# Kernel tuning notes

Hardware: AMD Instinct MI355X
Metric: run time of the kernel (lower is better)

## Reference

```python
import jax, jax.numpy as jnp
import numpy as np

B, TV, TL = 4, 13600, 256
VD, LD, E, H = 256, 768, 256, 8
HD = E // H
SCALE = HD ** -0.5
CLAMP = 50000.0
NEG = -9e15


def _xavier(k, out_d, in_d):
    lim = np.sqrt(6.0 / (in_d + out_d)).astype(np.float32)
    return jax.random.uniform(k, (out_d, in_d), minval=-lim, maxval=lim, dtype=jnp.float32)


def setup_inputs() -> dict:
    key = jax.random.key(0)
    ks = jax.random.split(key, 10)
    return {
        "v": jax.random.normal(ks[0], (B, TV, VD), dtype=jnp.float32),
        "l": jax.random.normal(ks[1], (B, TL, LD), dtype=jnp.float32),
        "v_pos": jax.random.normal(ks[2], (B, TV, VD), dtype=jnp.float32),
        "attention_mask_v": jnp.ones((B, TV), dtype=jnp.float32),
        "attention_mask_l": jnp.ones((B, TL), dtype=jnp.float32),
        "Wq": _xavier(ks[3], E, VD), "bq": jnp.zeros((E,), jnp.float32),
        "Wk": _xavier(ks[4], E, LD), "bk": jnp.zeros((E,), jnp.float32),
        "Wvv": _xavier(ks[5], E, VD), "bvv": jnp.zeros((E,), jnp.float32),
        "Wvl": _xavier(ks[6], E, LD), "bvl": jnp.zeros((E,), jnp.float32),
        "Wov": _xavier(ks[7], VD, E), "bov": jnp.zeros((VD,), jnp.float32),
        "Wol": _xavier(ks[8], LD, E), "bol": jnp.zeros((LD,), jnp.float32),
    }


def _heads(x):  # [B, T, E] -> [B, H, T, HD]
    b, t, _ = x.shape
    return x.reshape(b, t, H, HD).transpose(0, 2, 1, 3)


def reference(v, l, v_pos, attention_mask_v, attention_mask_l,
              Wq, bq, Wk, bk, Wvv, bvv, Wvl, bvl, Wov, bov, Wol, bol):
    # projections (eval mode: dropout disabled)
    q = _heads(((v + v_pos) @ Wq.T + bq) * SCALE)        # [B,H,TV,HD]
    k = _heads(l @ Wk.T + bk)                             # [B,H,TL,HD]
    val_v = _heads(v @ Wvv.T + bvv)                       # [B,H,TV,HD]
    val_l = _heads(l @ Wvl.T + bvl)                       # [B,H,TL,HD]

    # shared scores, computed once: [B,H,TV,TL]
    aw = jnp.einsum('bhtd,bhsd->bhts', q, k)
    aw = jnp.clip(aw, -CLAMP, CLAMP)

    # language-direction scores: transpose, stabilize, clamp
    aw_l = aw.transpose(0, 1, 3, 2)                       # [B,H,TL,TV]
    aw_l = aw_l - jnp.max(aw_l, axis=-1, keepdims=True)
    aw_l = jnp.clip(aw_l, -CLAMP, CLAMP)
    # torch masked_fill(mask==0, NEG) then + : nonzero mask values are ADDED
    mv = jnp.where(attention_mask_v == 0, NEG, attention_mask_v)[:, None, None, :]
    aw_l = aw_l + mv
    p_l = jax.nn.softmax(aw_l, axis=-1)

    # vision-direction scores
    ml = jnp.where(attention_mask_l == 0, NEG, attention_mask_l)[:, None, None, :]
    p_v = jax.nn.softmax(aw + ml, axis=-1)

    out_v = jnp.einsum('bhts,bhsd->bhtd', p_v, val_l)     # [B,H,TV,HD]
    out_l = jnp.einsum('bhst,bhtd->bhsd', p_l, val_v)     # [B,H,TL,HD]
    out_v = out_v.transpose(0, 2, 1, 3).reshape(B, TV, E) @ Wov.T + bov
    out_l = out_l.transpose(0, 2, 1, 3).reshape(B, TL, E) @ Wol.T + bol
    return (out_v, out_l)
```

## Files before the change

kernel.cpp:

```cpp
#include <hip/hip_runtime.h>
#include <math.h>


typedef unsigned short u16;
typedef unsigned int   u32;
typedef __attribute__((ext_vector_type(2))) u32 u32x2;
typedef __attribute__((ext_vector_type(4))) u16 us4;
typedef __attribute__((ext_vector_type(8))) u16 us8;
typedef __attribute__((ext_vector_type(8))) short s8b;
typedef __attribute__((ext_vector_type(4))) float f4;

#define B_   4
#define TV_  13600
#define TL_  256
#define VD_  256
#define LD_  768
#define E_   256
#define H_   8
#define HD_  32
#define PREC 36

static constexpr float SCALE_  = 0.17677669529663687f;
static constexpr float NEG_    = -9e15f;
static constexpr float LOG2E_  = 1.4426950408889634f;

__device__ __forceinline__ float bf2f(u16 x) {
    return __uint_as_float(((u32)x) << 16);
}
__device__ __forceinline__ u16 f2bf(float f) {
    u32 u = __float_as_uint(f);
    u += 0x7fffu + ((u >> 16) & 1u);
    return (u16)(u >> 16);
}
__device__ __forceinline__ u32 cvtpk(float lo, float hi) {
    u32 r;
    asm("v_cvt_pk_bf16_f32 %0, %1, %2" : "=v"(r) : "v"(lo), "v"(hi));
    return r;
}
__device__ __forceinline__ float bflo(u32 w) { return __uint_as_float(w << 16); }
__device__ __forceinline__ float bfhi(u32 w) { return __uint_as_float(w & 0xffff0000u); }

__device__ __forceinline__ s8b frag32(const u16* base, int row, int q) {
    int slot = q ^ ((row >> 1) & 3);
    return *(const s8b*)(base + row * 32 + slot * 8);
}

__global__ void sniff_kernel(const void* __restrict__ mask, int* __restrict__ flag) {
    if (threadIdx.x == 0 && blockIdx.x == 0) {
        u32 w = *(const u32*)mask;
        *flag = (w == 0x3F800000u) ? 1 : 0;
    }
}

__global__ __launch_bounds__(256) void prep_v_kernel(
    const int* __restrict__ flag, const void* __restrict__ v,
    const void* __restrict__ vp, u16* __restrict__ vb, u16* __restrict__ vqb)
{
    const bool f32 = (*flag != 0);
    const size_t n = (size_t)B_ * TV_ * VD_;
    size_t i = ((size_t)blockIdx.x * 256 + threadIdx.x) * 4;
    const size_t stride = (size_t)gridDim.x * 256 * 4;
    for (; i < n; i += stride) {
        float a[4], b[4];
        if (f32) {
            float4 x = ((const float4*)v)[i >> 2];
            float4 y = ((const float4*)vp)[i >> 2];
            a[0]=x.x; a[1]=x.y; a[2]=x.z; a[3]=x.w;
            b[0]=y.x; b[1]=y.y; b[2]=y.z; b[3]=y.w;
        } else {
            us4 x = ((const us4*)v)[i >> 2];
            us4 y = ((const us4*)vp)[i >> 2];
            #pragma unroll
            for (int j = 0; j < 4; ++j) { a[j]=bf2f(x[j]); b[j]=bf2f(y[j]); }
        }
        us4 o1, o2;
        #pragma unroll
        for (int j = 0; j < 4; ++j) { o1[j]=f2bf(a[j]); o2[j]=f2bf(a[j]+b[j]); }
        ((us4*)vb)[i >> 2] = o1;
        ((us4*)vqb)[i >> 2] = o2;
    }
}

struct Seg { const void* src; void* dst; int n; int toF32; };
struct PrepArgs { Seg s[13]; };

__global__ __launch_bounds__(256) void prep_rest_kernel(
    const int* __restrict__ flag, PrepArgs args)
{
    const bool f32 = (*flag != 0);
    for (int k = 0; k < 13; ++k) {
        Seg sg = args.s[k];
        for (int j = blockIdx.x * 256 + threadIdx.x; j < sg.n;
             j += gridDim.x * 256) {
            float x = f32 ? ((const float*)sg.src)[j] : bf2f(((const u16*)sg.src)[j]);
            if (sg.toF32) ((float*)sg.dst)[j] = x;
            else          ((u16*)sg.dst)[j]   = f2bf(x);
        }
    }
}

template<bool CEXT>
__global__ __launch_bounds__(256) void gemm_mfma(
    const int* __restrict__ flag,
    const u16* __restrict__ A, const u16* __restrict__ W,
    const float* __restrict__ bias, void* __restrict__ C, size_t c_off,
    int N, int K, float scale)
{
    __shared__ __align__(16) u16 As[128 * 32];
    __shared__ __align__(16) u16 Bs[128 * 32];
    const int tid  = threadIdx.x;
    const int lane = tid & 63, wid = tid >> 6;
    const int wm = wid >> 1, wn = wid & 1;
    const size_t m0 = (size_t)blockIdx.x * 128;
    const int n0 = blockIdx.y * 128;

    const int srow = tid >> 1;
    const int half = tid & 1;
    const int ssw  = (srow >> 1) & 3;
    const int sl0  = half * 2, sl1 = half * 2 + 1;

    f4 acc[4][4];
    #pragma unroll
    for (int i = 0; i < 4; ++i)
        #pragma unroll
        for (int j = 0; j < 4; ++j) acc[i][j] = (f4){0.f, 0.f, 0.f, 0.f};

    for (int k0 = 0; k0 < K; k0 += 32) {
        {
            const u16* ga = A + (m0 + srow) * (size_t)K + k0;
            *(us8*)&As[srow*32 + sl0*8] = *(const us8*)(ga + (sl0 ^ ssw) * 8);
            *(us8*)&As[srow*32 + sl1*8] = *(const us8*)(ga + (sl1 ^ ssw) * 8);
            const u16* gb = W + ((size_t)(n0 + srow)) * (size_t)K + k0;
            *(us8*)&Bs[srow*32 + sl0*8] = *(const us8*)(gb + (sl0 ^ ssw) * 8);
            *(us8*)&Bs[srow*32 + sl1*8] = *(const us8*)(gb + (sl1 ^ ssw) * 8);
        }
        __syncthreads();
        s8b af[4], bf[4];
        const int q = lane >> 4;
        #pragma unroll
        for (int mt = 0; mt < 4; ++mt)
            af[mt] = frag32(As, wm*64 + mt*16 + (lane & 15), q);
        #pragma unroll
        for (int nt = 0; nt < 4; ++nt)
            bf[nt] = frag32(Bs, wn*64 + nt*16 + (lane & 15), q);
        __builtin_amdgcn_s_setprio(1);
        #pragma unroll
        for (int mt = 0; mt < 4; ++mt)
            #pragma unroll
            for (int nt = 0; nt < 4; ++nt)
                acc[mt][nt] = __builtin_amdgcn_mfma_f32_16x16x32_bf16(
                    af[mt], bf[nt], acc[mt][nt], 0, 0, 0);
        __builtin_amdgcn_s_setprio(0);
        __syncthreads();
    }

    const int q = lane >> 4;
    const bool f32out = CEXT ? (*flag != 0) : false;
    #pragma unroll
    for (int nt = 0; nt < 4; ++nt) {
        const int col = n0 + wn*64 + nt*16 + (lane & 15);
        const float bv = bias[col];
        #pragma unroll
        for (int mt = 0; mt < 4; ++mt) {
            #pragma unroll
            for (int reg = 0; reg < 4; ++reg) {
                const size_t row = m0 + wm*64 + mt*16 + q*4 + reg;
                const float val = (acc[mt][nt][reg] + bv) * scale;
                const size_t idx = c_off + row * (size_t)N + col;
                if (CEXT && f32out) ((float*)C)[idx] = val;
                else                ((u16*)C)[idx]   = f2bf(val);
            }
        }
    }
}

__global__ __launch_bounds__(256, 4) void attn_v_mfma(
    const int* __restrict__ flag,
    const u16* __restrict__ qm, const u16* __restrict__ km,
    const u16* __restrict__ vm, const void* __restrict__ maskl,
    u16* __restrict__ outm)
{
    __shared__ __align__(16) u16 Qs[64 * 32];
    __shared__ __align__(16) u16 Ks[256 * 32];
    __shared__ __align__(16) u16 VTs[32 * 264];
    __shared__ float mls[256];

    const int tid = threadIdx.x, lane = tid & 63, wid = tid >> 6;
    const int bb = blockIdx.z, hh = blockIdx.y;
    const int t0 = blockIdx.x * 64;
    const int q  = lane >> 4;
    const int l15 = lane & 15;

    {
        int row = tid >> 2, slot = tid & 3;
        int sw = (row >> 1) & 3;
        int tg = t0 + row; if (tg >= TV_) tg = TV_ - 1;
        const u16* gp = qm + ((size_t)(bb*TV_ + tg)) * E_ + hh*HD_;
        *(us8*)&Qs[row*32 + slot*8] = *(const us8*)(gp + ((slot ^ sw) * 8));
    }
    {
        int s = tid, sw = (s >> 1) & 3;
        const u16* gp = km + ((size_t)(bb*TL_ + s)) * E_ + hh*HD_;
        #pragma unroll
        for (int slot = 0; slot < 4; ++slot)
            *(us8*)&Ks[s*32 + slot*8] = *(const us8*)(gp + ((slot ^ sw) * 8));
    }
    {
        int s = tid;
        const u16* gp = vm + ((size_t)(bb*TL_ + s)) * E_ + hh*HD_;
        #pragma unroll
        for (int d0 = 0; d0 < 32; d0 += 8) {
            us8 vv = *(const us8*)(gp + d0);
            #pragma unroll
            for (int j = 0; j < 8; ++j) VTs[(d0 + j)*264 + s] = vv[j];
        }
        float mv = (*flag) ? ((const float*)maskl)[(size_t)bb*TL_ + s]
                           : bf2f(((const u16*)maskl)[(size_t)bb*TL_ + s]);
        mls[s] = (mv == 0.0f) ? NEG_ : mv;
    }
    __syncthreads();

    const s8b qf = frag32(Qs, wid*16 + l15, q);
    f4 sacc[16];
    __builtin_amdgcn_s_setprio(1);
    #pragma unroll
    for (int mt = 0; mt < 16; ++mt) {
        s8b kf = frag32(Ks, mt*16 + l15, q);
        f4 z = {0.f, 0.f, 0.f, 0.f};
        sacc[mt] = __builtin_amdgcn_mfma_f32_16x16x32_bf16(kf, qf, z, 0, 0, 0);
    }
    __builtin_amdgcn_s_setprio(0);

    float vmax = -1e30f;
    #pragma unroll
    for (int mt = 0; mt < 16; ++mt) {
        f4 mv4 = *(const f4*)&mls[mt*16 + q*4];
        #pragma unroll
        for (int r = 0; r < 4; ++r) {
            float v = sacc[mt][r] + mv4[r];
            sacc[mt][r] = v;
            vmax = fmaxf(vmax, v);
        }
    }
    vmax = fmaxf(vmax, __shfl_xor(vmax, 16));
    vmax = fmaxf(vmax, __shfl_xor(vmax, 32));

    const float nmL = -vmax * LOG2E_;
    float sum = 0.f;
    u32 pw[32];
    #pragma unroll
    for (int mt = 0; mt < 16; ++mt) {
        float p0 = exp2f(fmaf(sacc[mt][0], LOG2E_, nmL));
        float p1 = exp2f(fmaf(sacc[mt][1], LOG2E_, nmL));
        float p2 = exp2f(fmaf(sacc[mt][2], LOG2E_, nmL));
        float p3 = exp2f(fmaf(sacc[mt][3], LOG2E_, nmL));
        u32 w0 = cvtpk(p0, p1), w1 = cvtpk(p2, p3);
        pw[2*mt]   = w0;
        pw[2*mt+1] = w1;
        sum += bflo(w0) + bfhi(w0) + bflo(w1) + bfhi(w1);
    }
    sum += __shfl_xor(sum, 16);
    sum += __shfl_xor(sum, 32);
    float Lreg[4];
    #pragma unroll
    for (int r = 0; r < 4; ++r) Lreg[r] = __shfl(sum, q*4 + r);

    __syncthreads();

    u16* myP = Ks + wid * (16 * 40);
    f4 oacc[2];
    oacc[0] = (f4){0.f,0.f,0.f,0.f};
    oacc[1] = (f4){0.f,0.f,0.f,0.f};
    __builtin_amdgcn_s_setprio(1);
    #pragma unroll
    for (int ks = 0; ks < 8; ++ks) {
        *(u32x2*)&myP[l15*40 + q*4]      = (u32x2){pw[4*ks],   pw[4*ks+1]};
        *(u32x2*)&myP[l15*40 + 16 + q*4] = (u32x2){pw[4*ks+2], pw[4*ks+3]};
        s8b pa = *(const s8b*)&myP[l15*40 + q*8];
        #pragma unroll
        for (int nt = 0; nt < 2; ++nt) {
            s8b vb = *(const s8b*)&VTs[(nt*16 + l15)*264 + ks*32 + q*8];
            oacc[nt] = __builtin_amdgcn_mfma_f32_16x16x32_bf16(pa, vb, oacc[nt], 0, 0, 0);
        }
    }
    __builtin_amdgcn_s_setprio(0);

    #pragma unroll
    for (int r = 0; r < 4; ++r) {
        const int tg = t0 + wid*16 + q*4 + r;
        if (tg < TV_) {
            const float inv = 1.0f / Lreg[r];
            #pragma unroll
            for (int nt = 0; nt < 2; ++nt)
                outm[((size_t)(bb*TV_ + tg)) * E_ + hh*HD_ + nt*16 + l15] =
                    f2bf(oacc[nt][r] * inv);
        }
    }
}

__global__ __launch_bounds__(256, 8) void attn_l_mfma(
    const int* __restrict__ flag,
    const u16* __restrict__ qm, const u16* __restrict__ km,
    const u16* __restrict__ vm, const void* __restrict__ maskv,
    u16* __restrict__ part, int nchunk, int chunk)
{
    __shared__ __align__(16) u16 smem0[128 * 40];
    __shared__ __align__(16) u16 Qs[32 * 32];
    __shared__ __align__(16) u16 VTs[32 * 32];
    __shared__ float mvs[32];

    const int tid = threadIdx.x, lane = tid & 63, wid = tid >> 6;
    const int bb = blockIdx.z, hh = blockIdx.y;
    const int tc  = blockIdx.x >> 1;
    const int s0b = (blockIdx.x & 1) * 128;
    const int q = lane >> 4, l15 = lane & 15;
    const bool f32m = (*flag != 0);

    {
        int row = tid >> 1, half = tid & 1;
        int sw = (row >> 1) & 3;
        const u16* gp = km + ((size_t)(bb*TL_ + s0b + row)) * E_ + hh*HD_;
        int sl0 = half*2, sl1 = half*2 + 1;
        *(us8*)&smem0[row*32 + sl0*8] = *(const us8*)(gp + ((sl0 ^ sw) * 8));
        *(us8*)&smem0[row*32 + sl1*8] = *(const us8*)(gp + ((sl1 ^ sw) * 8));
    }
    s8b bk0 = frag32(smem0, wid*32 + l15, q);
    s8b bk1 = frag32(smem0, wid*32 + 16 + l15, q);

    float m_s[2], l_s[2];
    f4 oacc[2][2];
    m_s[0] = m_s[1] = -1e30f;
    l_s[0] = l_s[1] = 0.f;
    oacc[0][0] = oacc[0][1] = oacc[1][0] = oacc[1][1] = (f4){0.f,0.f,0.f,0.f};

    const int nstep = chunk >> 5;
    for (int step = 0; step < nstep; ++step) {
        const int t0 = tc * chunk + step * 32;
        if (tid < 128) {
            int row = tid >> 2, slot = tid & 3;
            int sw = (row >> 1) & 3;
            const u16* gp = qm + ((size_t)(bb*TV_ + t0 + row)) * E_ + hh*HD_;
            *(us8*)&Qs[row*32 + slot*8] = *(const us8*)(gp + ((slot ^ sw) * 8));
        } else {
            int t2 = tid - 128;
            int trow = t2 >> 2, d0 = (t2 & 3) * 8;
            us8 vv = *(const us8*)(vm + ((size_t)(bb*TV_ + t0 + trow)) * E_ + hh*HD_ + d0);
            #pragma unroll
            for (int j = 0; j < 8; ++j) {
                int d = d0 + j;
                VTs[d*32 + (((trow >> 3) ^ ((d >> 1) & 3)) * 8) + (trow & 7)] = vv[j];
            }
        }
        if (tid < 32) {
            float mv = f32m ? ((const float*)maskv)[(size_t)bb*TV_ + t0 + tid]
                            : bf2f(((const u16*)maskv)[(size_t)bb*TV_ + t0 + tid]);
            mvs[tid] = (mv == 0.0f) ? NEG_ : mv;
        }
        __syncthreads();

        s8b aq0 = frag32(Qs, l15, q);
        s8b aq1 = frag32(Qs, 16 + l15, q);
        f4 sacc[2][2];
        __builtin_amdgcn_s_setprio(1);
        {
            f4 zz = {0.f, 0.f, 0.f, 0.f};
            sacc[0][0] = __builtin_amdgcn_mfma_f32_16x16x32_bf16(aq0, bk0, zz, 0, 0, 0);
            sacc[0][1] = __builtin_amdgcn_mfma_f32_16x16x32_bf16(aq0, bk1, zz, 0, 0, 0);
            sacc[1][0] = __builtin_amdgcn_mfma_f32_16x16x32_bf16(aq1, bk0, zz, 0, 0, 0);
            sacc[1][1] = __builtin_amdgcn_mfma_f32_16x16x32_bf16(aq1, bk1, zz, 0, 0, 0);
        }
        __builtin_amdgcn_s_setprio(0);

        float mvq[2][4];
        #pragma unroll
        for (int tt = 0; tt < 2; ++tt)
            #pragma unroll
            for (int r = 0; r < 4; ++r) mvq[tt][r] = mvs[tt*16 + q*4 + r];

        #pragma unroll
        for (int st = 0; st < 2; ++st) {
            float v[2][4];
            float vmax = -1e30f;
            #pragma unroll
            for (int tt = 0; tt < 2; ++tt)
                #pragma unroll
                for (int r = 0; r < 4; ++r) {
                    v[tt][r] = sacc[tt][st][r] + mvq[tt][r];
                    vmax = fmaxf(vmax, v[tt][r]);
                }
            vmax = fmaxf(vmax, __shfl_xor(vmax, 16));
            vmax = fmaxf(vmax, __shfl_xor(vmax, 32));
            float m = m_s[st];
            if (__any(vmax > m + 8.0f)) {
                float nm = fmaxf(m, vmax);
                float al = exp2f((m - nm) * LOG2E_);
                l_s[st] *= al;
                #pragma unroll
                for (int dt = 0; dt < 2; ++dt)
                    #pragma unroll
                    for (int r = 0; r < 4; ++r) oacc[dt][st][r] *= al;
                m_s[st] = m = nm;
            }
            const float nmL = -m * LOG2E_;
            const int ls = wid*32 + st*16 + l15;
            float ps = 0.f;
            #pragma unroll
            for (int tt = 0; tt < 2; ++tt) {
                float p0 = exp2f(fmaf(v[tt][0], LOG2E_, nmL));
                float p1 = exp2f(fmaf(v[tt][1], LOG2E_, nmL));
                float p2 = exp2f(fmaf(v[tt][2], LOG2E_, nmL));
                float p3 = exp2f(fmaf(v[tt][3], LOG2E_, nmL));
                u32 w0 = cvtpk(p0, p1), w1 = cvtpk(p2, p3);
                *(u32x2*)&smem0[ls*40 + tt*16 + q*4] = (u32x2){w0, w1};
                ps += bflo(w0) + bfhi(w0) + bflo(w1) + bfhi(w1);
            }
            ps += __shfl_xor(ps, 16);
            ps += __shfl_xor(ps, 32);
            l_s[st] += ps;
        }

        s8b av0 = frag32(VTs, l15, q);
        s8b av1 = frag32(VTs, 16 + l15, q);
        __builtin_amdgcn_s_setprio(1);
        #pragma unroll
        for (int st = 0; st < 2; ++st) {
            s8b bp = *(const s8b*)&smem0[(wid*32 + st*16 + l15)*40 + q*8];
            oacc[0][st] = __builtin_amdgcn_mfma_f32_16x16x32_bf16(av0, bp, oacc[0][st], 0, 0, 0);
            oacc[1][st] = __builtin_amdgcn_mfma_f32_16x16x32_bf16(av1, bp, oacc[1][st], 0, 0, 0);
        }
        __builtin_amdgcn_s_setprio(0);
        __syncthreads();
    }

    #pragma unroll
    for (int st = 0; st < 2; ++st) {
        const int s = s0b + wid*32 + st*16 + l15;
        u16* rec = part + ((size_t)((bb*H_ + hh)*TL_ + s) * nchunk + tc) * PREC;
        #pragma unroll
        for (int dt = 0; dt < 2; ++dt)
            #pragma unroll
            for (int r = 0; r < 4; ++r)
                rec[dt*16 + q*4 + r] = f2bf(oacc[dt][st][r]);
        if (q == 0) {
            *(float*)(rec + 32) = m_s[st];
            *(float*)(rec + 34) = l_s[st];
        }
    }
}

__global__ __launch_bounds__(256) void attn_l_merge(
    const u16* __restrict__ part, u16* __restrict__ outm, int nchunk)
{
    const int R = blockIdx.x * 8 + (threadIdx.x >> 5);
    const int d = threadIdx.x & 31;
    const u16* rec0 = part + (size_t)R * nchunk * PREC;
    float m = -1e30f;
    for (int c = 0; c < nchunk; ++c)
        m = fmaxf(m, *(const float*)(rec0 + c*PREC + 32));
    float L = 0.f, o = 0.f;
    for (int c = 0; c < nchunk; ++c) {
        float mc = *(const float*)(rec0 + c*PREC + 32);
        float lc = *(const float*)(rec0 + c*PREC + 34);
        float w  = exp2f((mc - m) * LOG2E_);
        L += lc * w;
        o += bf2f(rec0[c*PREC + d]) * w;
    }
    o /= L;
    const int bb = R >> 11, hh = (R >> 8) & 7, ss = R & 255;
    outm[(size_t)(bb*TL_ + ss) * E_ + hh*HD_ + d] = f2bf(o);
}

extern "C" void kernel_launch(void* const* d_in, const int* in_sizes, int n_in,
                              void* d_out, int out_size, void* d_ws, size_t ws_size,
                              hipStream_t stream)
{
    const void* v     = d_in[0];
    const void* l     = d_in[1];
    const void* vpos  = d_in[2];
    const void* maskv = d_in[3];
    const void* maskl = d_in[4];
    const void* Wq  = d_in[5];   const void* bq  = d_in[6];
    const void* Wk  = d_in[7];   const void* bk  = d_in[8];
    const void* Wvv = d_in[9];   const void* bvv = d_in[10];
    const void* Wvl = d_in[11];  const void* bvl = d_in[12];
    const void* Wov = d_in[13];  const void* bov = d_in[14];
    const void* Wol = d_in[15];  const void* bol = d_in[16];

    const size_t BIG   = (size_t)B_*TV_*E_*2;
    const size_t TLBUF = (size_t)B_*TL_*E_*2;
    const size_t LBUF  = (size_t)B_*TL_*LD_*2;
    auto part_bytes = [](int nc) { return (size_t)B_*H_*TL_ * (size_t)nc * (PREC*2); };

    const size_t fixed = 512 + 2*(BIG+256) + (LBUF+256) + 3*(TLBUF+256)
                       + (131072+256)*3 + (393216+256)*3 + (8192+256);
    const int cand[3] = {25, 17, 5};
    int nchunk = 5;
    for (int i = 0; i < 3; ++i)
        if (fixed + part_bytes(cand[i]) + 256 <= ws_size) { nchunk = cand[i]; break; }
    const int chunk = TV_ / nchunk;

    char* ws = (char*)d_ws;
    size_t off = 0;
    auto carve = [&](size_t bytes) -> char* {
        char* p = ws + off;
        off += (bytes + 255) & ~(size_t)255;
        return p;
    };
    int*   flag    = (int*)carve(512);
    u16*   slot1   = (u16*)carve(BIG);
    u16*   slot2   = (u16*)carve(BIG);
    u16*   lb      = (u16*)carve(LBUF);
    u16*   k_ws    = (u16*)carve(TLBUF);
    u16*   vall_ws = (u16*)carve(TLBUF);
    u16*   attnl_ws= (u16*)carve(TLBUF);
    u16*   wqb     = (u16*)carve(131072);
    u16*   wkb     = (u16*)carve(393216);
    u16*   wvvb    = (u16*)carve(131072);
    u16*   wvlb    = (u16*)carve(393216);
    u16*   wovb    = (u16*)carve(131072);
    u16*   wolb    = (u16*)carve(393216);
    float* biasf   = (float*)carve(8192);
    u16*   part_ws = (u16*)carve(part_bytes(nchunk));

    u16* vb    = slot1;
    u16* vqb   = slot2;
    u16* valv  = slot2;
    u16* attnv = slot1;
    u16* q_ws  = (u16*)d_out;

    float* bqf  = biasf;        float* bkf  = biasf + 256;
    float* bvvf = biasf + 512;  float* bvlf = biasf + 768;
    float* bovf = biasf + 1024; float* bolf = biasf + 1280;

    const dim3 blk(256);
    const size_t outl_off = (size_t)B_*TV_*VD_;

    sniff_kernel<<<1, 64, 0, stream>>>(maskv, flag);

    prep_v_kernel<<<2048, blk, 0, stream>>>(flag, v, vpos, vb, vqb);
    PrepArgs pa;
    pa.s[0]  = { l,   lb,   B_*TL_*LD_, 0 };
    pa.s[1]  = { Wq,  wqb,  E_*VD_,     0 };
    pa.s[2]  = { Wk,  wkb,  E_*LD_,     0 };
    pa.s[3]  = { Wvv, wvvb, E_*VD_,     0 };
    pa.s[4]  = { Wvl, wvlb, E_*LD_,     0 };
    pa.s[5]  = { Wov, wovb, VD_*E_,     0 };
    pa.s[6]  = { Wol, wolb, LD_*E_,     0 };
    pa.s[7]  = { bq,  bqf,  E_,  1 };
    pa.s[8]  = { bk,  bkf,  E_,  1 };
    pa.s[9]  = { bvv, bvvf, E_,  1 };
    pa.s[10] = { bvl, bvlf, E_,  1 };
    pa.s[11] = { bov, bovf, VD_, 1 };
    pa.s[12] = { bol, bolf, LD_, 1 };
    prep_rest_kernel<<<256, blk, 0, stream>>>(flag, pa);

    gemm_mfma<false><<<dim3(425, 2), blk, 0, stream>>>(flag, vqb, wqb,  bqf,  q_ws,    0, E_, VD_, SCALE_);
    gemm_mfma<false><<<dim3(425, 2), blk, 0, stream>>>(flag, vb,  wvvb, bvvf, valv,    0, E_, VD_, 1.0f);
    gemm_mfma<false><<<dim3(8,   2), blk, 0, stream>>>(flag, lb,  wkb,  bkf,  k_ws,    0, E_, LD_, 1.0f);
    gemm_mfma<false><<<dim3(8,   2), blk, 0, stream>>>(flag, lb,  wvlb, bvlf, vall_ws, 0, E_, LD_, 1.0f);

    attn_l_mfma <<<dim3(nchunk*2, H_, B_), blk, 0, stream>>>(flag, q_ws, k_ws, valv, maskv, part_ws, nchunk, chunk);
    attn_l_merge<<<dim3(B_*H_*TL_/8),      blk, 0, stream>>>(part_ws, attnl_ws, nchunk);
    attn_v_mfma <<<dim3((TV_+63)/64, H_, B_), blk, 0, stream>>>(flag, q_ws, k_ws, vall_ws, maskl, attnv);

    gemm_mfma<true><<<dim3(425, 2), blk, 0, stream>>>(flag, attnv,    wovb, bovf, d_out, 0,        VD_, E_, 1.0f);
    gemm_mfma<true><<<dim3(8,   6), blk, 0, stream>>>(flag, attnl_ws, wolb, bolf, d_out, outl_off, LD_, E_, 1.0f);
}
```

Baseline: 478.1 us.

## Store projections head-major and widen attn_l blocks to all 256 keys

The projection GEMMs now write Q, K and the value tensors in a [B,H,T,HD] head-major layout, so the attention kernels read contiguous 64-byte rows per head instead of strided slices of the E dimension. attn_l_mfma now has each block cover all 256 language rows (four 16-row tiles per wave) instead of splitting them across two blocks. This halves redundant Q/V tile loads, at the cost of more registers and LDS per block and lower occupancy (launch bounds drop from 8 to 4). Partial results are split into a packed bf16 output array and a separate float2 max/sum array laid out chunk-major, so both the stores and the merge reads are coalesced.

Measured after the change: 454.7 us. -4.9%, faster.

```diff
diff --git a/kernel.cpp b/kernel.cpp
--- a/kernel.cpp
+++ b/kernel.cpp
@@ -18,7 +18,7 @@
 #define E_   256
 #define H_   8
 #define HD_  32
-#define PREC 36
+#define NREC (B_*H_*TL_)
 
 static constexpr float SCALE_  = 0.17677669529663687f;
 static constexpr float NEG_    = -9e15f;
@@ -99,7 +99,7 @@
     }
 }
 
-template<bool CEXT>
+template<int OMODE, int TDIM>
 __global__ __launch_bounds__(256) void gemm_mfma(
     const int* __restrict__ flag,
     const u16* __restrict__ A, const u16* __restrict__ W,
@@ -155,7 +155,7 @@
     }
 
     const int q = lane >> 4;
-    const bool f32out = CEXT ? (*flag != 0) : false;
+    const bool f32out = (OMODE == 1) ? (*flag != 0) : false;
     #pragma unroll
     for (int nt = 0; nt < 4; ++nt) {
         const int col = n0 + wn*64 + nt*16 + (lane & 15);
@@ -164,11 +164,17 @@
         for (int mt = 0; mt < 4; ++mt) {
             #pragma unroll
             for (int reg = 0; reg < 4; ++reg) {
-                const size_t row = m0 + wm*64 + mt*16 + q*4 + reg;
+                const int row = (int)m0 + wm*64 + mt*16 + q*4 + reg;
                 const float val = (acc[mt][nt][reg] + bv) * scale;
-                const size_t idx = c_off + row * (size_t)N + col;
-                if (CEXT && f32out) ((float*)C)[idx] = val;
-                else                ((u16*)C)[idx]   = f2bf(val);
+                if (OMODE == 2) {
+                    const int b = row / TDIM, t = row - b * TDIM;
+                    ((u16*)C)[(((size_t)(b*H_ + (col >> 5)))*TDIM + t)*HD_ + (col & 31)]
+                        = f2bf(val);
+                } else {
+                    const size_t idx = c_off + (size_t)row * N + col;
+                    if (f32out) ((float*)C)[idx] = val;
+                    else        ((u16*)C)[idx]   = f2bf(val);
+                }
             }
         }
     }
@@ -187,6 +193,7 @@
 
     const int tid = threadIdx.x, lane = tid & 63, wid = tid >> 6;
     const int bb = blockIdx.z, hh = blockIdx.y;
+    const int bh = bb*H_ + hh;
     const int t0 = blockIdx.x * 64;
     const int q  = lane >> 4;
     const int l15 = lane & 15;
@@ -195,19 +202,19 @@
         int row = tid >> 2, slot = tid & 3;
         int sw = (row >> 1) & 3;
         int tg = t0 + row; if (tg >= TV_) tg = TV_ - 1;
-        const u16* gp = qm + ((size_t)(bb*TV_ + tg)) * E_ + hh*HD_;
+        const u16* gp = qm + ((size_t)(bh*TV_ + tg)) * HD_;
         *(us8*)&Qs[row*32 + slot*8] = *(const us8*)(gp + ((slot ^ sw) * 8));
     }
     {
         int s = tid, sw = (s >> 1) & 3;
-        const u16* gp = km + ((size_t)(bb*TL_ + s)) * E_ + hh*HD_;
+        const u16* gp = km + ((size_t)(bh*TL_ + s)) * HD_;
         #pragma unroll
         for (int slot = 0; slot < 4; ++slot)
             *(us8*)&Ks[s*32 + slot*8] = *(const us8*)(gp + ((slot ^ sw) * 8));
     }
     {
         int s = tid;
-        const u16* gp = vm + ((size_t)(bb*TL_ + s)) * E_ + hh*HD_;
+        const u16* gp = vm + ((size_t)(bh*TL_ + s)) * HD_;
         #pragma unroll
         for (int d0 = 0; d0 < 32; d0 += 8) {
             us8 vv = *(const us8*)(gp + d0);
@@ -298,40 +305,44 @@
     }
 }
 
-__global__ __launch_bounds__(256, 8) void attn_l_mfma(
+__global__ __launch_bounds__(256, 4) void attn_l_mfma(
     const int* __restrict__ flag,
     const u16* __restrict__ qm, const u16* __restrict__ km,
     const u16* __restrict__ vm, const void* __restrict__ maskv,
-    u16* __restrict__ part, int nchunk, int chunk)
-{
-    __shared__ __align__(16) u16 smem0[128 * 40];
+    u16* __restrict__ part_o, float2* __restrict__ part_ml,
+    int nchunk, int chunk)
+{
+    __shared__ __align__(16) u16 smem0[256 * 40];
     __shared__ __align__(16) u16 Qs[32 * 32];
     __shared__ __align__(16) u16 VTs[32 * 32];
     __shared__ float mvs[32];
 
     const int tid = threadIdx.x, lane = tid & 63, wid = tid >> 6;
-    const int bb = blockIdx.z, hh = blockIdx.y;
-    const int tc  = blockIdx.x >> 1;
-    const int s0b = (blockIdx.x & 1) * 128;
+    const int bb = blockIdx.z, hh = blockIdx.y, tc = blockIdx.x;
+    const int bh = bb*H_ + hh;
     const int q = lane >> 4, l15 = lane & 15;
     const bool f32m = (*flag != 0);
 
     {
-        int row = tid >> 1, half = tid & 1;
-        int sw = (row >> 1) & 3;
-        const u16* gp = km + ((size_t)(bb*TL_ + s0b + row)) * E_ + hh*HD_;
-        int sl0 = half*2, sl1 = half*2 + 1;
-        *(us8*)&smem0[row*32 + sl0*8] = *(const us8*)(gp + ((sl0 ^ sw) * 8));
-        *(us8*)&smem0[row*32 + sl1*8] = *(const us8*)(gp + ((sl1 ^ sw) * 8));
-    }
-    s8b bk0 = frag32(smem0, wid*32 + l15, q);
-    s8b bk1 = frag32(smem0, wid*32 + 16 + l15, q);
-
-    float m_s[2], l_s[2];
-    f4 oacc[2][2];
-    m_s[0] = m_s[1] = -1e30f;
-    l_s[0] = l_s[1] = 0.f;
-    oacc[0][0] = oacc[0][1] = oacc[1][0] = oacc[1][1] = (f4){0.f,0.f,0.f,0.f};
+        int s = tid, sw = (s >> 1) & 3;
+        const u16* gp = km + ((size_t)(bh*TL_ + s)) * HD_;
+        #pragma unroll
+        for (int slot = 0; slot < 4; ++slot)
+            *(us8*)&smem0[s*32 + slot*8] = *(const us8*)(gp + ((slot ^ sw) * 8));
+    }
+    s8b bk[4];
+    #pragma unroll
+    for (int st = 0; st < 4; ++st)
+        bk[st] = frag32(smem0, wid*64 + st*16 + l15, q);
+
+    float m_s[4], l_s[4];
+    f4 oacc[2][4];
+    #pragma unroll
+    for (int st = 0; st < 4; ++st) {
+        m_s[st] = -1e30f; l_s[st] = 0.f;
+        oacc[0][st] = (f4){0.f,0.f,0.f,0.f};
+        oacc[1][st] = (f4){0.f,0.f,0.f,0.f};
+    }
 
     const int nstep = chunk >> 5;
     for (int step = 0; step < nstep; ++step) {
@@ -339,12 +350,12 @@
         if (tid < 128) {
             int row = tid >> 2, slot = tid & 3;
             int sw = (row >> 1) & 3;
-            const u16* gp = qm + ((size_t)(bb*TV_ + t0 + row)) * E_ + hh*HD_;
+            const u16* gp = qm + ((size_t)(bh*TV_ + t0 + row)) * HD_;
             *(us8*)&Qs[row*32 + slot*8] = *(const us8*)(gp + ((slot ^ sw) * 8));
         } else {
             int t2 = tid - 128;
             int trow = t2 >> 2, d0 = (t2 & 3) * 8;
-            us8 vv = *(const us8*)(vm + ((size_t)(bb*TV_ + t0 + trow)) * E_ + hh*HD_ + d0);
+            us8 vv = *(const us8*)(vm + ((size_t)(bh*TV_ + t0 + trow)) * HD_ + d0);
             #pragma unroll
             for (int j = 0; j < 8; ++j) {
                 int d = d0 + j;
@@ -360,14 +371,13 @@
 
         s8b aq0 = frag32(Qs, l15, q);
         s8b aq1 = frag32(Qs, 16 + l15, q);
-        f4 sacc[2][2];
+        f4 sacc[2][4];
         __builtin_amdgcn_s_setprio(1);
-        {
+        #pragma unroll
+        for (int st = 0; st < 4; ++st) {
             f4 zz = {0.f, 0.f, 0.f, 0.f};
-            sacc[0][0] = __builtin_amdgcn_mfma_f32_16x16x32_bf16(aq0, bk0, zz, 0, 0, 0);
-            sacc[0][1] = __builtin_amdgcn_mfma_f32_16x16x32_bf16(aq0, bk1, zz, 0, 0, 0);
-            sacc[1][0] = __builtin_amdgcn_mfma_f32_16x16x32_bf16(aq1, bk0, zz, 0, 0, 0);
-            sacc[1][1] = __builtin_amdgcn_mfma_f32_16x16x32_bf16(aq1, bk1, zz, 0, 0, 0);
+            sacc[0][st] = __builtin_amdgcn_mfma_f32_16x16x32_bf16(aq0, bk[st], zz, 0, 0, 0);
+            sacc[1][st] = __builtin_amdgcn_mfma_f32_16x16x32_bf16(aq1, bk[st], zz, 0, 0, 0);
         }
         __builtin_amdgcn_s_setprio(0);
 
@@ -378,7 +388,7 @@
             for (int r = 0; r < 4; ++r) mvq[tt][r] = mvs[tt*16 + q*4 + r];
 
         #pragma unroll
-        for (int st = 0; st < 2; ++st) {
+        for (int st = 0; st < 4; ++st) {
             float v[2][4];
             float vmax = -1e30f;
             #pragma unroll
@@ -402,7 +412,7 @@
                 m_s[st] = m = nm;
             }
             const float nmL = -m * LOG2E_;
-            const int ls = wid*32 + st*16 + l15;
+            const int ls = wid*64 + st*16 + l15;
             float ps = 0.f;
             #pragma unroll
             for (int tt = 0; tt < 2; ++tt) {
@@ -423,8 +433,8 @@
         s8b av1 = frag32(VTs, 16 + l15, q);
         __builtin_amdgcn_s_setprio(1);
         #pragma unroll
-        for (int st = 0; st < 2; ++st) {
-            s8b bp = *(const s8b*)&smem0[(wid*32 + st*16 + l15)*40 + q*8];
+        for (int st = 0; st < 4; ++st) {
+            s8b bp = *(const s8b*)&smem0[(wid*64 + st*16 + l15)*40 + q*8];
             oacc[0][st] = __builtin_amdgcn_mfma_f32_16x16x32_bf16(av0, bp, oacc[0][st], 0, 0, 0);
             oacc[1][st] = __builtin_amdgcn_mfma_f32_16x16x32_bf16(av1, bp, oacc[1][st], 0, 0, 0);
         }
@@ -433,37 +443,38 @@
     }
 
     #pragma unroll
-    for (int st = 0; st < 2; ++st) {
-        const int s = s0b + wid*32 + st*16 + l15;
-        u16* rec = part + ((size_t)((bb*H_ + hh)*TL_ + s) * nchunk + tc) * PREC;
-        #pragma unroll
-        for (int dt = 0; dt < 2; ++dt)
-            #pragma unroll
-            for (int r = 0; r < 4; ++r)
-                rec[dt*16 + q*4 + r] = f2bf(oacc[dt][st][r]);
+    for (int st = 0; st < 4; ++st) {
+        const int s = wid*64 + st*16 + l15;
+        const size_t R = (size_t)bh*TL_ + s;
+        u16* ro = part_o + ((size_t)tc*NREC + R)*32;
+        u32 w0 = cvtpk(oacc[0][st][0], oacc[0][st][1]);
+        u32 w1 = cvtpk(oacc[0][st][2], oacc[0][st][3]);
+        u32 w2 = cvtpk(oacc[1][st][0], oacc[1][st][1]);
+        u32 w3 = cvtpk(oacc[1][st][2], oacc[1][st][3]);
+        *(u32x2*)&ro[q*4]      = (u32x2){w0, w1};
+        *(u32x2*)&ro[16 + q*4] = (u32x2){w2, w3};
         if (q == 0) {
-            *(float*)(rec + 32) = m_s[st];
-            *(float*)(rec + 34) = l_s[st];
+            float2 mlv; mlv.x = m_s[st]; mlv.y = l_s[st];
+            part_ml[(size_t)tc*NREC + R] = mlv;
         }
     }
 }
 
 __global__ __launch_bounds__(256) void attn_l_merge(
-    const u16* __restrict__ part, u16* __restrict__ outm, int nchunk)
+    const u16* __restrict__ part_o, const float2* __restrict__ part_ml,
+    u16* __restrict__ outm, int nchunk)
 {
     const int R = blockIdx.x * 8 + (threadIdx.x >> 5);
     const int d = threadIdx.x & 31;
-    const u16* rec0 = part + (size_t)R * nchunk * PREC;
     float m = -1e30f;
     for (int c = 0; c < nchunk; ++c)
-        m = fmaxf(m, *(const float*)(rec0 + c*PREC + 32));
+        m = fmaxf(m, part_ml[(size_t)c*NREC + R].x);
     float L = 0.f, o = 0.f;
     for (int c = 0; c < nchunk; ++c) {
-        float mc = *(const float*)(rec0 + c*PREC + 32);
-        float lc = *(const float*)(rec0 + c*PREC + 34);
-        float w  = exp2f((mc - m) * LOG2E_);
-        L += lc * w;
-        o += bf2f(rec0[c*PREC + d]) * w;
+        float2 mlv = part_ml[(size_t)c*NREC + R];
+        float w = exp2f((mlv.x - m) * LOG2E_);
+        L += mlv.y * w;
+        o += bf2f(part_o[((size_t)c*NREC + R)*32 + d]) * w;
     }
     o /= L;
     const int bb = R >> 11, hh = (R >> 8) & 7, ss = R & 255;
@@ -489,14 +500,14 @@
     const size_t BIG   = (size_t)B_*TV_*E_*2;
     const size_t TLBUF = (size_t)B_*TL_*E_*2;
     const size_t LBUF  = (size_t)B_*TL_*LD_*2;
-    auto part_bytes = [](int nc) { return (size_t)B_*H_*TL_ * (size_t)nc * (PREC*2); };
+    auto part_bytes = [](int nc) { return (size_t)NREC * (size_t)nc * 72; };
 
     const size_t fixed = 512 + 2*(BIG+256) + (LBUF+256) + 3*(TLBUF+256)
                        + (131072+256)*3 + (393216+256)*3 + (8192+256);
     const int cand[3] = {25, 17, 5};
     int nchunk = 5;
     for (int i = 0; i < 3; ++i)
-        if (fixed + part_bytes(cand[i]) + 256 <= ws_size) { nchunk = cand[i]; break; }
+        if (fixed + part_bytes(cand[i]) + 512 <= ws_size) { nchunk = cand[i]; break; }
     const int chunk = TV_ / nchunk;
 
     char* ws = (char*)d_ws;
@@ -520,7 +531,8 @@
     u16*   wovb    = (u16*)carve(131072);
     u16*   wolb    = (u16*)carve(393216);
     float* biasf   = (float*)carve(8192);
-    u16*   part_ws = (u16*)carve(part_bytes(nchunk));
+    u16*    part_o  = (u16*)carve((size_t)nchunk*NREC*64);
+    float2* part_ml = (float2*)carve((size_t)nchunk*NREC*8);
 
     u16* vb    = slot1;
     u16* vqb   = slot2;
@@ -554,15 +566,15 @@
     pa.s[12] = { bol, bolf, LD_, 1 };
     prep_rest_kernel<<<256, blk, 0, stream>>>(flag, pa);
 
-    gemm_mfma<false><<<dim3(425, 2), blk, 0, stream>>>(flag, vqb, wqb,  bqf,  q_ws,    0, E_, VD_, SCALE_);
-    gemm_mfma<false><<<dim3(425, 2), blk, 0, stream>>>(flag, vb,  wvvb, bvvf, valv,    0, E_, VD_, 1.0f);
-    gemm_mfma<false><<<dim3(8,   2), blk, 0, stream>>>(flag, lb,  wkb,  bkf,  k_ws,    0, E_, LD_, 1.0f);
-    gemm_mfma<false><<<dim3(8,   2), blk, 0, stream>>>(flag, lb,  wvlb, bvlf, vall_ws, 0, E_, LD_, 1.0f);
-
-    attn_l_mfma <<<dim3(nchunk*2, H_, B_), blk, 0, stream>>>(flag, q_ws, k_ws, valv, maskv, part_ws, nchunk, chunk);
-    attn_l_merge<<<dim3(B_*H_*TL_/8),      blk, 0, stream>>>(part_ws, attnl_ws, nchunk);
+    gemm_mfma<2, TV_><<<dim3(425, 2), blk, 0, stream>>>(flag, vqb, wqb,  bqf,  q_ws,    0, E_, VD_, SCALE_);
+    gemm_mfma<2, TV_><<<dim3(425, 2), blk, 0, stream>>>(flag, vb,  wvvb, bvvf, valv,    0, E_, VD_, 1.0f);
+    gemm_mfma<2, TL_><<<dim3(8,   2), blk, 0, stream>>>(flag, lb,  wkb,  bkf,  k_ws,    0, E_, LD_, 1.0f);
+    gemm_mfma<2, TL_><<<dim3(8,   2), blk, 0, stream>>>(flag, lb,  wvlb, bvlf, vall_ws, 0, E_, LD_, 1.0f);
+
+    attn_l_mfma <<<dim3(nchunk, H_, B_), blk, 0, stream>>>(flag, q_ws, k_ws, valv, maskv, part_o, part_ml, nchunk, chunk);
+    attn_l_merge<<<dim3(B_*H_*TL_/8),    blk, 0, stream>>>(part_o, part_ml, attnl_ws, nchunk);
     attn_v_mfma <<<dim3((TV_+63)/64, H_, B_), blk, 0, stream>>>(flag, q_ws, k_ws, vall_ws, maskl, attnv);
 
-    gemm_mfma<true><<<dim3(425, 2), blk, 0, stream>>>(flag, attnv,    wovb, bovf, d_out, 0,        VD_, E_, 1.0f);
-    gemm_mfma<true><<<dim3(8,   6), blk, 0, stream>>>(flag, attnl_ws, wolb, bolf, d_out, outl_off, LD_, E_, 1.0f);
-}
+    gemm_mfma<1, 1><<<dim3(425, 2), blk, 0, stream>>>(flag, attnv,    wovb, bovf, d_out, 0,        VD_, E_, 1.0f);
+    gemm_mfma<1, 1><<<dim3(8,   6), blk, 0, stream>>>(flag, attnl_ws, wolb, bolf, d_out, outl_off, LD_, E_, 1.0f);
+}
```
